# Optimization experiments

Hardware: AMD Instinct MI355X
Metric: run time of the kernel (lower is better)

Reference implementation:

```python
import jax, jax.numpy as jnp
import numpy as np

EPS = 1e-5  # torch LayerNorm default


def _ln(v, g, b):
    m = jnp.mean(v, axis=-1, keepdims=True)
    var = jnp.var(v, axis=-1, keepdims=True)
    return (v - m) / jnp.sqrt(var + EPS) * g + b


def setup_inputs() -> dict:
    key = jax.random.key(0)
    ks = jax.random.split(key, 12)
    S, E, H = 4096, 1024, 8
    s = 0.02  # weight scale ~ nn.Linear init magnitude
    return {
        "x": jax.random.normal(ks[0], (S, E), jnp.float32),
        "Wq": jax.random.normal(ks[1], (H, E, E), jnp.float32) * s,
        "bq": jax.random.normal(ks[2], (H, E), jnp.float32) * s,
        "Wk": jax.random.normal(ks[3], (H, E, E), jnp.float32) * s,
        "bk": jax.random.normal(ks[4], (H, E), jnp.float32) * s,
        "Wv": jax.random.normal(ks[5], (H, E, E), jnp.float32) * s,
        "bv": jax.random.normal(ks[6], (H, E), jnp.float32) * s,
        "Wz": jax.random.normal(ks[7], (E, H * E), jnp.float32) * s,
        "bz": jax.random.normal(ks[8], (E,), jnp.float32) * s,
        "g1": jnp.ones((E,), jnp.float32),
        "b1": jnp.zeros((E,), jnp.float32),
        "Wf": jax.random.normal(ks[9], (E, E), jnp.float32) * s,
        "bf": jax.random.normal(ks[10], (E,), jnp.float32) * s,
        "g2": jnp.ones((E,), jnp.float32),
        "b2": jnp.zeros((E,), jnp.float32),
    }


def reference(x, Wq, bq, Wk, bk, Wv, bv, Wz, bz, g1, b1, Wf, bf, g2, b2):
    S, E = x.shape
    # per-head projections, batched over heads: y_h = x @ W_h.T + b_h
    Q = jnp.einsum('se,hoe->hso', x, Wq) + bq[:, None, :]  # [H,S,E]
    K = jnp.einsum('se,hoe->hso', x, Wk) + bk[:, None, :]
    V = jnp.einsum('se,hoe->hso', x, Wv) + bv[:, None, :]
    # non-standard attention: scores = K^T @ Q over the sequence dim -> [H,E,E]
    scores = jnp.einsum('hse,hsf->hef', K, Q) / jnp.sqrt(jnp.float32(E))
    A = jax.nn.softmax(scores, axis=-1)  # torch softmax(dim=1) on [E,E]
    Zh = jnp.einsum('hse,hef->hsf', V, A)  # [H,S,E]
    # concat heads along feature dim -> [S, H*E]
    Z = jnp.transpose(Zh, (1, 0, 2)).reshape(S, -1)
    O = Z @ Wz.T + bz
    LN1 = _ln(O, g1, b1) + x
    FN = LN1 @ Wf.T + bf
    LN2 = _ln(FN, g2, b2) + LN1
    return LN2
```

## Files before the change

kernel.cpp:

```cpp
#include <hip/hip_runtime.h>

#define S_DIM 4096
#define E_DIM 1024
#define H_DIM 8

typedef __bf16 bf16x8 __attribute__((ext_vector_type(8)));
typedef float  f32x4  __attribute__((ext_vector_type(4)));

__device__ __forceinline__ void async16(const __bf16* gsrc, __bf16* lbase, int lane)
{
#if __has_builtin(__builtin_amdgcn_global_load_lds)
    __builtin_amdgcn_global_load_lds(
        (const __attribute__((address_space(1))) unsigned int*)gsrc,
        (__attribute__((address_space(3))) unsigned int*)lbase, 16, 0, 0);
#else
    ((int4*)lbase)[lane] = *(const int4*)gsrc;
#endif
}

template <int OUT, int AM, int BM>
__global__ __launch_bounds__(512, 1) void gemmP(
    const __bf16* __restrict__ Ag, const __bf16* __restrict__ Bg,
    void* __restrict__ Cg, int Klen, int kPerZ,
    int lda, int ldb, int ldc, long long sA, long long sB, long long sC,
    int nMt, int mtpx)
{
    __shared__ __bf16 sm[2 * 24576];

    const int tid  = threadIdx.x;
    const int lane = tid & 63;
    const int wave = tid >> 6;
    const int wm = wave >> 1, wn = wave & 1;
    const int t = lane & 15, q = lane >> 4;

    const int bid = blockIdx.x;
    const int bpz = nMt << 3;
    const int zi  = bid / bpz;
    const int rr  = bid - zi * bpz;
    int mt, nt;
    if (mtpx > 0) {
        const int xcd = rr & 7, s = rr >> 3;
        mt = xcd * mtpx + (s >> 3);
        nt = s & 7;
    } else {
        mt = rr >> 3;
        nt = rr & 7;
    }
    const int m0 = mt * 256;
    const int n0 = nt * 128;
    const int kbeg = zi * kPerZ;
    const int NT = Klen >> 6;

    const int gslot = ((lane & 7) ^ (lane >> 3)) & 7;
    const int lrow  = lane >> 3;

    auto stage_sub = [&](int kt, int which) {
        __bf16* base = &sm[(kt & 1) * 24576 + which * 8192 + wave * 512];
        const int kk = kbeg + kt * 64;
#pragma unroll
        for (int p = 0; p < 2; p++) {
            const int idx = p * 64 + wave * 8 + lrow;
            const __bf16* g;
            if (which == 2) {
                const int grow = n0 + idx;
                if constexpr (BM == 1)
                    g = Bg + (size_t)(m0 >> 10) * sB + (size_t)grow * ldb + kk + gslot * 8;
                else if constexpr (BM == 2)
                    g = Bg + (size_t)(kk >> 10) * sB + (size_t)grow * ldb + (kk & 1023) + gslot * 8;
                else
                    g = Bg + (size_t)grow * ldb + kk + gslot * 8;
            } else {
                const int grow = m0 + (((idx >> 5) << 6) | (idx & 31)) + (which ? 32 : 0);
                if constexpr (AM == 1)
                    g = Ag + (size_t)(m0 >> 10) * sA + (size_t)(grow & 1023) * lda + kk + gslot * 8;
                else if constexpr (AM == 2)
                    g = Ag + (size_t)(kk >> 10) * sA + (size_t)grow * lda + (kk & 1023) + gslot * 8;
                else
                    g = Ag + (size_t)grow * lda + kk + gslot * 8;
            }
            async16(g, base + p * 4096, lane);
        }
    };

    const int fx = t & 7;

    f32x4 acc[4][4];
#pragma unroll
    for (int i = 0; i < 4; i++)
#pragma unroll
        for (int j = 0; j < 4; j++) { f32x4 z = {0.f,0.f,0.f,0.f}; acc[i][j] = z; }

    stage_sub(0, 0); stage_sub(0, 2); stage_sub(0, 1);

    for (int kt = 0; kt < NT; ++kt) {
        const __bf16* ba = &sm[(kt & 1) * 24576];
        const __bf16* bb = ba + 8192;
        const __bf16* bB = ba + 16384;

        if (kt + 1 < NT) {
            stage_sub(kt + 1, 0); stage_sub(kt + 1, 2);
            asm volatile("s_waitcnt vmcnt(6)" ::: "memory");
        } else {
            asm volatile("s_waitcnt vmcnt(2)" ::: "memory");
        }
        __builtin_amdgcn_s_barrier();
        __builtin_amdgcn_sched_barrier(0);

        bf16x8 bfr[4][2], afr[2][2];
#pragma unroll
        for (int j = 0; j < 4; j++)
#pragma unroll
            for (int kk = 0; kk < 2; kk++)
                bfr[j][kk] = *(const bf16x8*)&bB[(wn*64 + j*16 + t) * 64 + (((kk<<2)|q) ^ fx) * 8];
#pragma unroll
        for (int i = 0; i < 2; i++)
#pragma unroll
            for (int kk = 0; kk < 2; kk++)
                afr[i][kk] = *(const bf16x8*)&ba[(wm*32 + i*16 + t) * 64 + (((kk<<2)|q) ^ fx) * 8];

        __builtin_amdgcn_s_setprio(1);
#pragma unroll
        for (int i = 0; i < 2; i++)
#pragma unroll
            for (int kk = 0; kk < 2; kk++)
#pragma unroll
                for (int j = 0; j < 4; j++)
                    acc[i][j] = __builtin_amdgcn_mfma_f32_16x16x32_bf16(afr[i][kk], bfr[j][kk], acc[i][j], 0, 0, 0);
        __builtin_amdgcn_s_setprio(0);
        __builtin_amdgcn_s_barrier();
        __builtin_amdgcn_sched_barrier(0);

        if (kt + 1 < NT) {
            stage_sub(kt + 1, 1);
            asm volatile("s_waitcnt vmcnt(6)" ::: "memory");
        } else {
            asm volatile("s_waitcnt vmcnt(0)" ::: "memory");
        }
        __builtin_amdgcn_s_barrier();
        __builtin_amdgcn_sched_barrier(0);

        bf16x8 afr2[2][2];
#pragma unroll
        for (int i = 0; i < 2; i++)
#pragma unroll
            for (int kk = 0; kk < 2; kk++)
                afr2[i][kk] = *(const bf16x8*)&bb[(wm*32 + i*16 + t) * 64 + (((kk<<2)|q) ^ fx) * 8];

        __builtin_amdgcn_s_setprio(1);
#pragma unroll
        for (int i = 0; i < 2; i++)
#pragma unroll
            for (int kk = 0; kk < 2; kk++)
#pragma unroll
                for (int j = 0; j < 4; j++)
                    acc[i+2][j] = __builtin_amdgcn_mfma_f32_16x16x32_bf16(afr2[i][kk], bfr[j][kk], acc[i+2][j], 0, 0, 0);
        __builtin_amdgcn_s_setprio(0);
        __builtin_amdgcn_s_barrier();
        __builtin_amdgcn_sched_barrier(0);
    }

#pragma unroll
    for (int i = 0; i < 4; i++) {
        const int rowb = m0 + wm * 64 + i * 16 + q * 4;
#pragma unroll
        for (int j = 0; j < 4; j++) {
            const int col = n0 + wn * 64 + j * 16 + t;
#pragma unroll
            for (int r = 0; r < 4; r++) {
                const float v = acc[i][j][r];
                if constexpr (OUT == 0) {
                    ((__bf16*)Cg)[(size_t)(rowb + r) * ldc + col] = (__bf16)v;
                } else {
                    float* C = (float*)Cg + (size_t)zi * sC;
                    C[(size_t)(rowb + r) * ldc + col] = v;
                }
            }
        }
    }
}

template <bool WN>
__global__ __launch_bounds__(256) void trans_cvt(
    const float* __restrict__ in, __bf16* __restrict__ outT,
    __bf16* __restrict__ outN, int R, int C)
{
    __shared__ float t[64][65];
    const size_t base = (size_t)blockIdx.z * R * C;
    const int r0 = blockIdx.y * 64, c0 = blockIdx.x * 64;
    const int tid = threadIdx.x;
    const int r = tid >> 2;
#pragma unroll
    for (int i = 0; i < 4; i++) {
        const int j = (tid & 3) + i * 4;
        float4 v = *(const float4*)(in + base + (size_t)(r0 + r) * C + c0 + j * 4);
        t[r][j*4+0] = v.x; t[r][j*4+1] = v.y; t[r][j*4+2] = v.z; t[r][j*4+3] = v.w;
        if constexpr (WN) {
            union { __bf16 h[4]; unsigned long long q; } u;
            u.h[0]=(__bf16)v.x; u.h[1]=(__bf16)v.y; u.h[2]=(__bf16)v.z; u.h[3]=(__bf16)v.w;
            *(unsigned long long*)(outN + base + (size_t)(r0 + r) * C + c0 + j * 4) = u.q;
        }
    }
    __syncthreads();
#pragma unroll
    for (int i = 0; i < 2; i++) {
        const int idx = tid + 256 * i;
        const int c = idx >> 3, h8 = idx & 7;
        union { __bf16 h[8]; int4 q; } u;
#pragma unroll
        for (int k = 0; k < 8; k++) u.h[k] = (__bf16)t[h8*8+k][c];
        *(int4*)(outT + base + (size_t)(c0 + c) * R + r0 + h8 * 8) = u.q;
    }
}

__global__ __launch_bounds__(256) void cvt_bf16(
    const float* __restrict__ in, __bf16* __restrict__ out)
{
    const size_t i = ((size_t)blockIdx.x * 256 + threadIdx.x) * 8;
    float4 a = *(const float4*)(in + i);
    float4 b = *(const float4*)(in + i + 4);
    union { __bf16 h[8]; int4 v; } u;
    u.h[0]=(__bf16)a.x; u.h[1]=(__bf16)a.y; u.h[2]=(__bf16)a.z; u.h[3]=(__bf16)a.w;
    u.h[4]=(__bf16)b.x; u.h[5]=(__bf16)b.y; u.h[6]=(__bf16)b.z; u.h[7]=(__bf16)b.w;
    *(int4*)(out + i) = u.v;
}

__global__ __launch_bounds__(256) void sum8_cvt(
    const float* __restrict__ P, __bf16* __restrict__ out)
{
    const size_t EE = (size_t)E_DIM * E_DIM;
    const size_t i = ((size_t)blockIdx.x * 256 + threadIdx.x) * 8;
    float4 a = {0.f,0.f,0.f,0.f}, b = {0.f,0.f,0.f,0.f};
#pragma unroll
    for (int p = 0; p < 8; p++) {
        float4 x = *(const float4*)(P + p*EE + i);
        float4 y = *(const float4*)(P + p*EE + i + 4);
        a.x+=x.x; a.y+=x.y; a.z+=x.z; a.w+=x.w;
        b.x+=y.x; b.y+=y.y; b.z+=y.z; b.w+=y.w;
    }
    union { __bf16 h[8]; int4 v; } u;
    u.h[0]=(__bf16)a.x; u.h[1]=(__bf16)a.y; u.h[2]=(__bf16)a.z; u.h[3]=(__bf16)a.w;
    u.h[4]=(__bf16)b.x; u.h[5]=(__bf16)b.y; u.h[6]=(__bf16)b.z; u.h[7]=(__bf16)b.w;
    *(int4*)(out + i) = u.v;
}

__global__ __launch_bounds__(256) void colsum_u(const float* __restrict__ x, float* __restrict__ u)
{
    const int c = threadIdx.x * 4;
    float4 a = {0.f,0.f,0.f,0.f};
    const int r0 = blockIdx.x * 64;
    for (int r = 0; r < 64; r++) {
        float4 v = *(const float4*)(x + (size_t)(r0 + r) * E_DIM + c);
        a.x += v.x; a.y += v.y; a.z += v.z; a.w += v.w;
    }
    atomicAdd(&u[c+0], a.x); atomicAdd(&u[c+1], a.y);
    atomicAdd(&u[c+2], a.z); atomicAdd(&u[c+3], a.w);
}

__global__ __launch_bounds__(256) void gemv_u(
    const float* __restrict__ Wk, const float* __restrict__ Wq,
    const float* __restrict__ u, float* __restrict__ kq, float* __restrict__ qq)
{
    const int gw = blockIdx.x * 4 + (threadIdx.x >> 6);
    const int lane = threadIdx.x & 63;
    const float* W = (gw < 8192) ? Wk + (size_t)gw * E_DIM
                                 : Wq + (size_t)(gw - 8192) * E_DIM;
    float s = 0.f;
#pragma unroll
    for (int i = 0; i < 4; i++) {
        float4 w = *(const float4*)(W + lane*16 + i*4);
        float4 z = *(const float4*)(u + lane*16 + i*4);
        s += w.x*z.x + w.y*z.y + w.z*z.z + w.w*z.w;
    }
#pragma unroll
    for (int o = 32; o > 0; o >>= 1) s += __shfl_down(s, o);
    if (lane == 0) { if (gw < 8192) kq[gw] = s; else qq[gw - 8192] = s; }
}

__global__ __launch_bounds__(256) void colsum_zb(
    const __bf16* __restrict__ Ab, const float* __restrict__ bv, float* __restrict__ zb)
{
    const int h = blockIdx.y;
    const int f = blockIdx.x * 256 + threadIdx.x;
    const int o0 = blockIdx.z * 256;
    const __bf16* A = Ab + (size_t)h * E_DIM * E_DIM + (size_t)o0 * E_DIM + f;
    const float* bvh = bv + h * E_DIM + o0;
    float s = 0.f;
    for (int o = 0; o < 256; o++) s += bvh[o] * (float)A[(size_t)o * E_DIM];
    atomicAdd(&zb[h * E_DIM + f], s);
}

__global__ __launch_bounds__(256) void gemv_oc(
    const float* __restrict__ Wz, const float* __restrict__ zb,
    const float* __restrict__ bz, float* __restrict__ oc)
{
    const int gw = blockIdx.x * 4 + (threadIdx.x >> 6);
    const int lane = threadIdx.x & 63;
    const float* W = Wz + (size_t)gw * (H_DIM * E_DIM);
    float s = 0.f;
#pragma unroll
    for (int i = 0; i < 32; i++) {
        float4 w = *(const float4*)(W + i*256 + lane*4);
        float4 z = *(const float4*)(zb + i*256 + lane*4);
        s += w.x*z.x + w.y*z.y + w.z*z.z + w.w*z.w;
    }
#pragma unroll
    for (int o = 32; o > 0; o >>= 1) s += __shfl_down(s, o);
    if (lane == 0) oc[gw] = s + bz[gw];
}

__global__ __launch_bounds__(256) void softmax_fused(
    const float* __restrict__ Sc, const float* __restrict__ kq,
    const float* __restrict__ qq, const float* __restrict__ bk,
    const float* __restrict__ bq, __bf16* __restrict__ Aout)
{
    __shared__ float red[4];
    const int row = blockIdx.x;
    const int h = row >> 10;
    const int tid = threadIdx.x, lane = tid & 63, wave = tid >> 6;
    const float kqj = kq[row], bkj = bk[row];
    const float cst = (float)S_DIM * bkj;

    float4 v = ((const float4*)(Sc + (size_t)row * E_DIM))[tid];
    const int c = tid * 4;
    float4 qv = *(const float4*)(qq + (h << 10) + c);
    float4 bv = *(const float4*)(bq + (h << 10) + c);
    v.x = (v.x + kqj*bv.x + bkj*qv.x + cst*bv.x) * 0.03125f;
    v.y = (v.y + kqj*bv.y + bkj*qv.y + cst*bv.y) * 0.03125f;
    v.z = (v.z + kqj*bv.z + bkj*qv.z + cst*bv.z) * 0.03125f;
    v.w = (v.w + kqj*bv.w + bkj*qv.w + cst*bv.w) * 0.03125f;

    float m = fmaxf(fmaxf(v.x, v.y), fmaxf(v.z, v.w));
#pragma unroll
    for (int o = 32; o > 0; o >>= 1) m = fmaxf(m, __shfl_down(m, o));
    if (lane == 0) red[wave] = m;
    __syncthreads();
    m = fmaxf(fmaxf(red[0], red[1]), fmaxf(red[2], red[3]));
    __syncthreads();

    const float e0 = __expf(v.x - m), e1 = __expf(v.y - m);
    const float e2 = __expf(v.z - m), e3 = __expf(v.w - m);
    float s = e0 + e1 + e2 + e3;
#pragma unroll
    for (int o = 32; o > 0; o >>= 1) s += __shfl_down(s, o);
    if (lane == 0) red[wave] = s;
    __syncthreads();
    s = red[0] + red[1] + red[2] + red[3];
    const float inv = 1.f / s;

    __bf16* out = Aout + (size_t)row * E_DIM + c;
    out[0] = (__bf16)(e0*inv); out[1] = (__bf16)(e1*inv);
    out[2] = (__bf16)(e2*inv); out[3] = (__bf16)(e3*inv);
}

template <int NPART, bool CB, bool WRITE_BF16>
__global__ __launch_bounds__(256) void ln_residual(
    const float* __restrict__ X, const float* __restrict__ cb,
    const float* __restrict__ resid,
    const float* __restrict__ g, const float* __restrict__ b,
    __bf16* __restrict__ outB, float* __restrict__ outF)
{
    __shared__ float redS[4], redQ[4];
    const int row = blockIdx.x;
    const int tid = threadIdx.x, lane = tid & 63, wave = tid >> 6;
    const size_t SE = (size_t)S_DIM * E_DIM;

    float4 v = ((const float4*)(X + (size_t)row * E_DIM))[tid];
#pragma unroll
    for (int p = 1; p < NPART; ++p) {
        float4 v1 = ((const float4*)(X + (size_t)p * SE + (size_t)row * E_DIM))[tid];
        v.x += v1.x; v.y += v1.y; v.z += v1.z; v.w += v1.w;
    }
    if constexpr (CB) {
        float4 cv = ((const float4*)cb)[tid];
        v.x += cv.x; v.y += cv.y; v.z += cv.z; v.w += cv.w;
    }
    float s = v.x + v.y + v.z + v.w;
    float q = v.x*v.x + v.y*v.y + v.z*v.z + v.w*v.w;
#pragma unroll
    for (int o = 32; o > 0; o >>= 1) { s += __shfl_down(s, o); q += __shfl_down(q, o); }
    if (lane == 0) { redS[wave] = s; redQ[wave] = q; }
    __syncthreads();
    s = redS[0]+redS[1]+redS[2]+redS[3];
    q = redQ[0]+redQ[1]+redQ[2]+redQ[3];

    const float mean = s * (1.f / E_DIM);
    const float var  = q * (1.f / E_DIM) - mean * mean;
    const float rstd = rsqrtf(var + 1e-5f);

    const int c0 = tid * 4;
    float4 rv = ((const float4*)(resid + (size_t)row * E_DIM))[tid];
    const float res[4] = {rv.x, rv.y, rv.z, rv.w};
    const float* vp = &v.x;
#pragma unroll
    for (int i = 0; i < 4; i++) {
        const float o = (vp[i] - mean) * rstd * g[c0+i] + b[c0+i] + res[i];
        outF[(size_t)row * E_DIM + c0 + i] = o;
        if constexpr (WRITE_BF16) outB[(size_t)row * E_DIM + c0 + i] = (__bf16)o;
    }
}

extern "C" void kernel_launch(void* const* d_in, const int* in_sizes, int n_in,
                              void* d_out, int out_size, void* d_ws, size_t ws_size,
                              hipStream_t stream)
{
    const float* x   = (const float*)d_in[0];
    const float* Wq  = (const float*)d_in[1];
    const float* bq  = (const float*)d_in[2];
    const float* Wk  = (const float*)d_in[3];
    const float* bk  = (const float*)d_in[4];
    const float* Wv  = (const float*)d_in[5];
    const float* bv  = (const float*)d_in[6];
    const float* Wz  = (const float*)d_in[7];
    const float* bz  = (const float*)d_in[8];
    const float* g1  = (const float*)d_in[9];
    const float* b1  = (const float*)d_in[10];
    const float* Wf  = (const float*)d_in[11];
    const float* bfp = (const float*)d_in[12];
    const float* g2  = (const float*)d_in[13];
    const float* b2  = (const float*)d_in[14];

    char* ws = (char*)d_ws;
    const long long EE = (long long)E_DIM * E_DIM;
    const long long SE = (long long)S_DIM * E_DIM;
    const size_t MB = 1024ull * 1024ull;

    __bf16* xb   = (__bf16*)(ws);
    __bf16* Wqb  = (__bf16*)(ws +   8*MB);
    __bf16* Wkb  = (__bf16*)(ws +  24*MB);
    __bf16* WvT  = (__bf16*)(ws +  40*MB);
    __bf16* Wzb  = (__bf16*)(ws +  56*MB);
    __bf16* Wfb  = (__bf16*)(ws +  72*MB);
    __bf16* Gb   = (__bf16*)(ws +  74*MB);
    __bf16* PTb  = (__bf16*)(ws +  76*MB);
    __bf16* xbT  = (__bf16*)(ws +  78*MB);
    float*  u    = (float*) (ws +  86*MB);
    float*  kq   = (float*) (ws +  86*MB +  65536);
    float*  qq   = (float*) (ws +  86*MB + 131072);
    float*  zb   = (float*) (ws +  86*MB + 196608);
    float*  oc   = (float*) (ws +  86*MB + 262144);
    __bf16* LN1b = (__bf16*)(ws +  87*MB);
    float*  LN1f = (float*) (ws +  95*MB);
    __bf16* Tb   = (__bf16*)(ws + 111*MB);
    float*  Sc   = (float*) (ws + 127*MB);
    __bf16* Ab   = (__bf16*)(ws + 159*MB);
    __bf16* Yb   = (__bf16*)(ws + 175*MB);
    float*  Gp   = (float*) (ws + 111*MB);
    float*  PTp  = (float*) (ws + 111*MB);
    float*  Ob   = (float*) (ws + 111*MB);
    float*  FNb  = (float*) (ws + 111*MB);

    dim3 blk(256);
    dim3 blk5(512);

    hipMemsetAsync(u,   0, E_DIM*4, stream);
    hipMemsetAsync(zb,  0, H_DIM*E_DIM*4, stream);

    trans_cvt<true><<<dim3(16, 64, 1), blk, 0, stream>>>(x, xbT, xb, S_DIM, E_DIM);
    cvt_bf16<<<dim3(4096), blk, 0, stream>>>(Wq, Wqb);
    cvt_bf16<<<dim3(4096), blk, 0, stream>>>(Wk, Wkb);
    cvt_bf16<<<dim3(4096), blk, 0, stream>>>(Wz, Wzb);
    cvt_bf16<<<dim3(512),  blk, 0, stream>>>(Wf, Wfb);
    trans_cvt<false><<<dim3(16, 16, 8), blk, 0, stream>>>(Wv, WvT, nullptr, E_DIM, E_DIM);

    colsum_u<<<dim3(64), blk, 0, stream>>>(x, u);
    gemv_u<<<dim3(4096), blk, 0, stream>>>(Wk, Wq, u, kq, qq);

    gemmP<1, 0, 0><<<dim3(256), blk5, 0, stream>>>(
        xbT, xbT, (void*)Gp, 512, 512, S_DIM, S_DIM, E_DIM, 0, 0, EE, 4, 0);
    sum8_cvt<<<dim3(512), blk, 0, stream>>>(Gp, Gb);

    gemmP<0, 0, 0><<<dim3(256), blk5, 0, stream>>>(
        Wkb, Gb, (void*)Tb, 1024, 0, E_DIM, E_DIM, E_DIM, 0, 0, 0, 32, 4);
    gemmP<1, 0, 1><<<dim3(256), blk5, 0, stream>>>(
        Tb, Wqb, (void*)Sc, 1024, 0, E_DIM, E_DIM, E_DIM, 0, EE, 0, 32, 4);
    softmax_fused<<<dim3(H_DIM * E_DIM), blk, 0, stream>>>(Sc, kq, qq, bk, bq, Ab);

    gemmP<0, 1, 1><<<dim3(256), blk5, 0, stream>>>(
        Wzb, Ab, (void*)Yb, 1024, 0, H_DIM * E_DIM, E_DIM, E_DIM, E_DIM, EE, 0, 32, 4);

    colsum_zb<<<dim3(4, 8, 4), blk, 0, stream>>>(Ab, bv, zb);
    gemv_oc<<<dim3(256), blk, 0, stream>>>(Wz, zb, bz, oc);

    gemmP<1, 2, 2><<<dim3(256), blk5, 0, stream>>>(
        Yb, WvT, (void*)PTp, 1024, 1024, E_DIM, E_DIM, E_DIM, EE, EE, EE, 4, 0);
    sum8_cvt<<<dim3(512), blk, 0, stream>>>(PTp, PTb);

    gemmP<1, 0, 0><<<dim3(256), blk5, 0, stream>>>(
        xb, PTb, (void*)Ob, 512, 512, E_DIM, E_DIM, E_DIM, 0, 0, SE, 16, 2);
    ln_residual<2, true, true><<<dim3(S_DIM), blk, 0, stream>>>(
        Ob, oc, x, g1, b1, LN1b, LN1f);

    gemmP<1, 0, 0><<<dim3(256), blk5, 0, stream>>>(
        LN1b, Wfb, (void*)FNb, 512, 512, E_DIM, E_DIM, E_DIM, 0, 0, SE, 16, 2);
    ln_residual<2, true, false><<<dim3(S_DIM), blk, 0, stream>>>(
        FNb, bfp, LN1f, g2, b2, nullptr, (float*)d_out);
}
```

Baseline: 453.6 us.

## Re-pipeline GEMM main loop and fuse preprocessing kernels

Restructures the gemmP k-loop so the next tile's sub-stages are issued after the LDS fragment reads for each MFMA half. This splits the B-fragment work into two halves and cuts one barrier per iteration, so global loads overlap MFMA compute better. Separately, the x column-sum moves into trans_cvt, the four weight conversions merge into one launch, and gemv_u reads the bf16 weights instead of fp32. gemv_u now uses bf16-rounded Wk/Wq, which slightly changes the precision of the bias-correction terms, and the reworked vmcnt/barrier ordering risks a race if the counts are wrong.

```diff
diff --git a/kernel.cpp b/kernel.cpp
--- a/kernel.cpp
+++ b/kernel.cpp
@@ -96,19 +96,15 @@
         const __bf16* ba = &sm[(kt & 1) * 24576];
         const __bf16* bb = ba + 8192;
         const __bf16* bB = ba + 16384;
-
-        if (kt + 1 < NT) {
-            stage_sub(kt + 1, 0); stage_sub(kt + 1, 2);
-            asm volatile("s_waitcnt vmcnt(6)" ::: "memory");
-        } else {
-            asm volatile("s_waitcnt vmcnt(2)" ::: "memory");
-        }
+        const bool more = (kt + 1 < NT);
+
+        asm volatile("s_waitcnt vmcnt(2)" ::: "memory");
         __builtin_amdgcn_s_barrier();
         __builtin_amdgcn_sched_barrier(0);
 
-        bf16x8 bfr[4][2], afr[2][2];
-#pragma unroll
-        for (int j = 0; j < 4; j++)
+        bf16x8 bfr[4][2], afr[2][2], afr2[2][2];
+#pragma unroll
+        for (int j = 0; j < 2; j++)
 #pragma unroll
             for (int kk = 0; kk < 2; kk++)
                 bfr[j][kk] = *(const bf16x8*)&bB[(wn*64 + j*16 + t) * 64 + (((kk<<2)|q) ^ fx) * 8];
@@ -117,6 +113,7 @@
 #pragma unroll
             for (int kk = 0; kk < 2; kk++)
                 afr[i][kk] = *(const bf16x8*)&ba[(wm*32 + i*16 + t) * 64 + (((kk<<2)|q) ^ fx) * 8];
+        if (more) stage_sub(kt + 1, 0);
 
         __builtin_amdgcn_s_setprio(1);
 #pragma unroll
@@ -124,27 +121,38 @@
 #pragma unroll
             for (int kk = 0; kk < 2; kk++)
 #pragma unroll
-                for (int j = 0; j < 4; j++)
+                for (int j = 0; j < 2; j++)
                     acc[i][j] = __builtin_amdgcn_mfma_f32_16x16x32_bf16(afr[i][kk], bfr[j][kk], acc[i][j], 0, 0, 0);
         __builtin_amdgcn_s_setprio(0);
+
+#pragma unroll
+        for (int j = 2; j < 4; j++)
+#pragma unroll
+            for (int kk = 0; kk < 2; kk++)
+                bfr[j][kk] = *(const bf16x8*)&bB[(wn*64 + j*16 + t) * 64 + (((kk<<2)|q) ^ fx) * 8];
+        if (more) stage_sub(kt + 1, 2);
+
+        __builtin_amdgcn_s_setprio(1);
+#pragma unroll
+        for (int i = 0; i < 2; i++)
+#pragma unroll
+            for (int kk = 0; kk < 2; kk++)
+#pragma unroll
+                for (int j = 2; j < 4; j++)
+                    acc[i][j] = __builtin_amdgcn_mfma_f32_16x16x32_bf16(afr[i][kk], bfr[j][kk], acc[i][j], 0, 0, 0);
+        __builtin_amdgcn_s_setprio(0);
+
+        if (more) asm volatile("s_waitcnt vmcnt(4)" ::: "memory");
+        else      asm volatile("s_waitcnt vmcnt(0)" ::: "memory");
         __builtin_amdgcn_s_barrier();
         __builtin_amdgcn_sched_barrier(0);
 
-        if (kt + 1 < NT) {
-            stage_sub(kt + 1, 1);
-            asm volatile("s_waitcnt vmcnt(6)" ::: "memory");
-        } else {
-            asm volatile("s_waitcnt vmcnt(0)" ::: "memory");
-        }
-        __builtin_amdgcn_s_barrier();
-        __builtin_amdgcn_sched_barrier(0);
-
-        bf16x8 afr2[2][2];
 #pragma unroll
         for (int i = 0; i < 2; i++)
 #pragma unroll
             for (int kk = 0; kk < 2; kk++)
                 afr2[i][kk] = *(const bf16x8*)&bb[(wm*32 + i*16 + t) * 64 + (((kk<<2)|q) ^ fx) * 8];
+        if (more) stage_sub(kt + 1, 1);
 
         __builtin_amdgcn_s_setprio(1);
 #pragma unroll
@@ -155,8 +163,6 @@
                 for (int j = 0; j < 4; j++)
                     acc[i+2][j] = __builtin_amdgcn_mfma_f32_16x16x32_bf16(afr2[i][kk], bfr[j][kk], acc[i+2][j], 0, 0, 0);
         __builtin_amdgcn_s_setprio(0);
-        __builtin_amdgcn_s_barrier();
-        __builtin_amdgcn_sched_barrier(0);
     }
 
 #pragma unroll
@@ -179,12 +185,13 @@
     }
 }
 
-template <bool WN>
+template <bool WN, bool CS>
 __global__ __launch_bounds__(256) void trans_cvt(
     const float* __restrict__ in, __bf16* __restrict__ outT,
-    __bf16* __restrict__ outN, int R, int C)
+    __bf16* __restrict__ outN, float* __restrict__ usum, int R, int C)
 {
     __shared__ float t[64][65];
+    __shared__ float cs[4][64];
     const size_t base = (size_t)blockIdx.z * R * C;
     const int r0 = blockIdx.y * 64, c0 = blockIdx.x * 64;
     const int tid = threadIdx.x;
@@ -210,17 +217,36 @@
         for (int k = 0; k < 8; k++) u.h[k] = (__bf16)t[h8*8+k][c];
         *(int4*)(outT + base + (size_t)(c0 + c) * R + r0 + h8 * 8) = u.q;
     }
-}
-
-__global__ __launch_bounds__(256) void cvt_bf16(
-    const float* __restrict__ in, __bf16* __restrict__ out)
-{
-    const size_t i = ((size_t)blockIdx.x * 256 + threadIdx.x) * 8;
+    if constexpr (CS) {
+        const int c = tid & 63, qg = tid >> 6;
+        float s = 0.f;
+#pragma unroll
+        for (int k = 0; k < 16; k++) s += t[qg*16 + k][c];
+        cs[qg][c] = s;
+        __syncthreads();
+        if (tid < 64)
+            atomicAdd(&usum[c0 + tid], cs[0][tid]+cs[1][tid]+cs[2][tid]+cs[3][tid]);
+    }
+}
+
+__global__ __launch_bounds__(256) void cvt_all(
+    const float* __restrict__ Wq, const float* __restrict__ Wk,
+    const float* __restrict__ Wz, const float* __restrict__ Wf,
+    __bf16* __restrict__ Wqb, __bf16* __restrict__ Wkb,
+    __bf16* __restrict__ Wzb, __bf16* __restrict__ Wfb)
+{
+    const int b = blockIdx.x;
+    const float* in; __bf16* out; int off;
+    if (b < 4096)       { in = Wq; out = Wqb; off = b; }
+    else if (b < 8192)  { in = Wk; out = Wkb; off = b - 4096; }
+    else if (b < 12288) { in = Wz; out = Wzb; off = b - 8192; }
+    else                { in = Wf; out = Wfb; off = b - 12288; }
+    const size_t i = ((size_t)off * 256 + threadIdx.x) * 8;
     float4 a = *(const float4*)(in + i);
-    float4 b = *(const float4*)(in + i + 4);
+    float4 c = *(const float4*)(in + i + 4);
     union { __bf16 h[8]; int4 v; } u;
     u.h[0]=(__bf16)a.x; u.h[1]=(__bf16)a.y; u.h[2]=(__bf16)a.z; u.h[3]=(__bf16)a.w;
-    u.h[4]=(__bf16)b.x; u.h[5]=(__bf16)b.y; u.h[6]=(__bf16)b.z; u.h[7]=(__bf16)b.w;
+    u.h[4]=(__bf16)c.x; u.h[5]=(__bf16)c.y; u.h[6]=(__bf16)c.z; u.h[7]=(__bf16)c.w;
     *(int4*)(out + i) = u.v;
 }
 
@@ -243,33 +269,22 @@
     *(int4*)(out + i) = u.v;
 }
 
-__global__ __launch_bounds__(256) void colsum_u(const float* __restrict__ x, float* __restrict__ u)
-{
-    const int c = threadIdx.x * 4;
-    float4 a = {0.f,0.f,0.f,0.f};
-    const int r0 = blockIdx.x * 64;
-    for (int r = 0; r < 64; r++) {
-        float4 v = *(const float4*)(x + (size_t)(r0 + r) * E_DIM + c);
-        a.x += v.x; a.y += v.y; a.z += v.z; a.w += v.w;
-    }
-    atomicAdd(&u[c+0], a.x); atomicAdd(&u[c+1], a.y);
-    atomicAdd(&u[c+2], a.z); atomicAdd(&u[c+3], a.w);
-}
-
 __global__ __launch_bounds__(256) void gemv_u(
-    const float* __restrict__ Wk, const float* __restrict__ Wq,
+    const __bf16* __restrict__ Wkb, const __bf16* __restrict__ Wqb,
     const float* __restrict__ u, float* __restrict__ kq, float* __restrict__ qq)
 {
     const int gw = blockIdx.x * 4 + (threadIdx.x >> 6);
     const int lane = threadIdx.x & 63;
-    const float* W = (gw < 8192) ? Wk + (size_t)gw * E_DIM
-                                 : Wq + (size_t)(gw - 8192) * E_DIM;
+    const __bf16* W = (gw < 8192) ? Wkb + (size_t)gw * E_DIM
+                                  : Wqb + (size_t)(gw - 8192) * E_DIM;
     float s = 0.f;
 #pragma unroll
-    for (int i = 0; i < 4; i++) {
-        float4 w = *(const float4*)(W + lane*16 + i*4);
-        float4 z = *(const float4*)(u + lane*16 + i*4);
-        s += w.x*z.x + w.y*z.y + w.z*z.z + w.w*z.w;
+    for (int i = 0; i < 2; i++) {
+        bf16x8 w = *(const bf16x8*)(W + lane*16 + i*8);
+        float4 z0 = *(const float4*)(u + lane*16 + i*8);
+        float4 z1 = *(const float4*)(u + lane*16 + i*8 + 4);
+        s += (float)w[0]*z0.x + (float)w[1]*z0.y + (float)w[2]*z0.z + (float)w[3]*z0.w
+           + (float)w[4]*z1.x + (float)w[5]*z1.y + (float)w[6]*z1.z + (float)w[7]*z1.w;
     }
 #pragma unroll
     for (int o = 32; o > 0; o >>= 1) s += __shfl_down(s, o);
@@ -455,15 +470,13 @@
     hipMemsetAsync(u,   0, E_DIM*4, stream);
     hipMemsetAsync(zb,  0, H_DIM*E_DIM*4, stream);
 
-    trans_cvt<true><<<dim3(16, 64, 1), blk, 0, stream>>>(x, xbT, xb, S_DIM, E_DIM);
-    cvt_bf16<<<dim3(4096), blk, 0, stream>>>(Wq, Wqb);
-    cvt_bf16<<<dim3(4096), blk, 0, stream>>>(Wk, Wkb);
-    cvt_bf16<<<dim3(4096), blk, 0, stream>>>(Wz, Wzb);
-    cvt_bf16<<<dim3(512),  blk, 0, stream>>>(Wf, Wfb);
-    trans_cvt<false><<<dim3(16, 16, 8), blk, 0, stream>>>(Wv, WvT, nullptr, E_DIM, E_DIM);
-
-    colsum_u<<<dim3(64), blk, 0, stream>>>(x, u);
-    gemv_u<<<dim3(4096), blk, 0, stream>>>(Wk, Wq, u, kq, qq);
+    trans_cvt<true, true><<<dim3(16, 64, 1), blk, 0, stream>>>(
+        x, xbT, xb, u, S_DIM, E_DIM);
+    cvt_all<<<dim3(12800), blk, 0, stream>>>(Wq, Wk, Wz, Wf, Wqb, Wkb, Wzb, Wfb);
+    trans_cvt<false, false><<<dim3(16, 16, 8), blk, 0, stream>>>(
+        Wv, WvT, nullptr, nullptr, E_DIM, E_DIM);
+
+    gemv_u<<<dim3(4096), blk, 0, stream>>>(Wkb, Wqb, u, kq, qq);
 
     gemmP<1, 0, 0><<<dim3(256), blk5, 0, stream>>>(
         xbT, xbT, (void*)Gp, 512, 512, S_DIM, S_DIM, E_DIM, 0, 0, EE, 4, 0);
```

After: 423.6 us. -6.6%, faster.
